# Kernel tuning notes

Measured on AMD Instinct MI355X. Metric: run time of the kernel, lower is better.

Reference implementation:

```python
import jax, jax.numpy as jnp
import numpy as np


def _lin_lrelu(x, W, b):
    # LinearBlock(c_in, c_out): Linear + LeakyReLU(0.01)
    return jax.nn.leaky_relu(x @ W + b)


def _mrconv(x_src, x_dst, edges, index_id, W, b):
    """BipartiteResMRConv: gather-diff-scatter_max + residual MLP.
    x_src: [B, Ns, C], x_dst: [B, Nd, C], edges: [2, E] int."""
    src = index_id[0][edges[0]]                     # [E]
    dst = index_id[0][edges[1]]                     # [E]
    diffs = x_dst[:, dst, :] - x_src[:, src, :]     # [B, E, C]
    d = jnp.swapaxes(diffs, 0, 1)                   # [E, B, C] (segment axis leading)
    m = jax.ops.segment_max(d, dst, num_segments=x_dst.shape[1])  # [Nd, B, C]
    m = jnp.where(jnp.isneginf(m), 0.0, m)          # empty segments -> 0 (maxes init zeros)
    maxes = jnp.swapaxes(m, 0, 1)                   # [B, Nd, C]
    h = jnp.concatenate([x_dst, maxes], axis=2)     # [B, Nd, 2C]
    return x_dst + _lin_lrelu(h, W, b)


def setup_inputs() -> dict:
    key = jax.random.key(0)
    ks = jax.random.split(key, 24)
    B, Nf, Ne, Nv, C = 4, 40000, 80000, 40000, 32
    E_fe, E_ev, E_ff, E_ef, E_ve = 160000, 160000, 240000, 160000, 160000

    def edges(k, E, ns, nd):
        k1, k2 = jax.random.split(k)
        return jnp.stack([jax.random.randint(k1, (E,), 0, ns),
                          jax.random.randint(k2, (E,), 0, nd)]).astype(jnp.int64)

    inp = {
        "x_f": jax.random.normal(ks[0], (B, Nf, 4), jnp.float32),
        "x_e": jax.random.normal(ks[1], (B, Ne, 6), jnp.float32),
        "x_v": jax.random.normal(ks[2], (B, Nv, 3), jnp.float32),
        "index_id": jnp.arange(max(Nf, Ne, Nv), dtype=jnp.int64)[None, :],
        "fe_edges": edges(ks[3], E_fe, Nf, Ne),
        "ev_edges": edges(ks[4], E_ev, Ne, Nv),
        "ff_edges": edges(ks[5], E_ff, Nf, Nf),
        "ef_edges": edges(ks[6], E_ef, Ne, Nf),
        "ve_edges": edges(ks[7], E_ve, Nv, Ne),
        "Wf": jax.random.normal(ks[8], (4, C), jnp.float32) * 0.1,
        "bf": jnp.zeros((C,), jnp.float32),
        "We": jax.random.normal(ks[9], (6, C), jnp.float32) * 0.1,
        "be": jnp.zeros((C,), jnp.float32),
        "Wv": jax.random.normal(ks[10], (3, C), jnp.float32) * 0.1,
        "bv": jnp.zeros((C,), jnp.float32),
    }
    for i, name in enumerate(["f2e", "e2v", "ff", "e2f", "v2e"]):
        inp[f"W_{name}"] = jax.random.normal(ks[11 + i], (2 * C, C), jnp.float32) * 0.1
        inp[f"b_{name}"] = jnp.zeros((C,), jnp.float32)
    return inp


def reference(x_f, x_e, x_v, index_id, fe_edges, ev_edges, ff_edges, ef_edges,
              ve_edges, Wf, bf, We, be, Wv, bv, W_f2e, b_f2e, W_e2v, b_e2v,
              W_ff, b_ff, W_e2f, b_e2f, W_v2e, b_v2e):
    xf0 = _lin_lrelu(x_f, Wf, bf)   # [B, Nf, 32]
    xe0 = _lin_lrelu(x_e, We, be)   # [B, Ne, 32]
    xv0 = _lin_lrelu(x_v, Wv, bv)   # [B, Nv, 32]
    xe = _mrconv(xf0, xe0, fe_edges, index_id, W_f2e, b_f2e)   # F2E
    xv = _mrconv(xe0, xv0, ev_edges, index_id, W_e2v, b_e2v)   # E2V
    xf = _mrconv(xf0, xf0, ff_edges, index_id, W_ff, b_ff)     # F2F (ffLayers)
    xf = _mrconv(xe, xf, ef_edges, index_id, W_e2f, b_e2f)     # E2F
    xe = _mrconv(xv, xe, ve_edges, index_id, W_v2e, b_v2e)     # V2E
    return (xf, xe, xv)
```

## Files before the change

### kernel.cpp

```cpp
#include <hip/hip_runtime.h>
#include <float.h>

#define LRELU(v) ((v) > 0.0f ? (v) : 0.01f * (v))

__device__ __forceinline__ int f2ord(float f) {
    int i = __float_as_int(f);
    return (i >= 0) ? i : (int)(0x80000000u - (unsigned int)i);
}
__device__ __forceinline__ float ord2f(int m) {
    int i = (m >= 0) ? m : (int)(0x80000000u - (unsigned int)m);
    return __int_as_float(i);
}

__global__ void prep(const float* __restrict__ xf, const float* __restrict__ xe,
                     const float* __restrict__ Wf, const float* __restrict__ bf,
                     const float* __restrict__ We, const float* __restrict__ be,
                     float* __restrict__ of, float* __restrict__ oe,
                     const int* __restrict__ e0, const int* __restrict__ e1,
                     const int* __restrict__ e2, const int* __restrict__ e3,
                     const int* __restrict__ e4, int* __restrict__ cur,
                     int* __restrict__ slots) {
    int bid = blockIdx.x;
    int t = threadIdx.x;
    if (bid < 15000) {
        int loc = bid * 256 + t;
        const int QF = 1280000;
        const float* x; const float* W; const float* bb; float* o; int cin;
        if (loc < QF) { x = xf; W = Wf; bb = bf; o = of; cin = 4; }
        else          { x = xe; W = We; bb = be; o = oe; cin = 6; loc -= QF; }
        int c0 = (loc & 7) * 4;
        int r  = loc >> 3;
        float4 acc = *(const float4*)(bb + c0);
        for (int k = 0; k < cin; ++k) {
            float xv_ = x[r * cin + k];
            float4 wv = *(const float4*)(W + k * 32 + c0);
            acc.x = fmaf(xv_, wv.x, acc.x); acc.y = fmaf(xv_, wv.y, acc.y);
            acc.z = fmaf(xv_, wv.z, acc.z); acc.w = fmaf(xv_, wv.w, acc.w);
        }
        float4 ov4;
        ov4.x = LRELU(acc.x); ov4.y = LRELU(acc.y);
        ov4.z = LRELU(acc.z); ov4.w = LRELU(acc.w);
        ((float4*)o)[loc] = ov4;
    } else {
        int idx = (bid - 15000) * 256 + t;
        if (idx >= 880000) return;
        const int cum[6]  = {0, 160000, 320000, 560000, 720000, 880000};
        const int bOff[5] = {0, 2500, 3750, 5000, 6250};
        const int Eg[5]   = {160000, 160000, 240000, 160000, 160000};
        const int* eds[5] = {e0, e1, e2, e3, e4};
        int g = 0;
#pragma unroll
        for (int k = 1; k < 5; ++k) g += (idx >= cum[k]);
        int e = idx - cum[g];
        int s = eds[g][e];
        int d = eds[g][Eg[g] + e];
        int cbase = (bOff[g] + (d >> 5)) * 8 + (idx & 7);
        int c = atomicAdd(&cur[cbase], 1);
        if (c < 64) slots[(size_t)cbase * 64 + c] = (s << 5) | (d & 31);
    }
}

struct ConvJob {
    const float* xsrc; const float* xdst;
    const int* cur; const int* slots;
    const float* W; const float* bias; float* out;
    const float* xraw; const float* Wlin; const float* blin;
    int Ns; int Nd; int blkStart; int cin;
};
struct ConvJobs { ConvJob e[3]; };

__global__ __launch_bounds__(256, 1)
void conv_fused(ConvJobs jobs) {
    __shared__ int smxi[128][33];
    int t = threadIdx.x;
    int bid = blockIdx.x;
    int g = (bid >= jobs.e[2].blkStart) ? 2 : (bid >= jobs.e[1].blkStart) ? 1 : 0;
    const float* xsrc  = jobs.e[g].xsrc;
    const float* xdst  = jobs.e[g].xdst;
    const int*   cur   = jobs.e[g].cur;
    const int*   slots = jobs.e[g].slots;
    const float* W     = jobs.e[g].W;
    const float* bias  = jobs.e[g].bias;
    float*       out   = jobs.e[g].out;
    const float* xraw  = jobs.e[g].xraw;
    const float* Wlin  = jobs.e[g].Wlin;
    const float* blin  = jobs.e[g].blin;
    int Ns = jobs.e[g].Ns, Nd = jobs.e[g].Nd;
    int cin = jobs.e[g].cin;
    int lb = bid - jobs.e[g].blkStart;
    int base = lb * 32;

    for (int i = t; i < 128 * 33; i += 256) ((int*)smxi)[i] = 0x7FFFFFFF;
    __syncthreads();

    int w    = t >> 6;
    int lane = t & 63;
    int r    = (w & 1) * 64 + lane;
    int c0   = __builtin_amdgcn_readfirstlane((w >> 1) * 16);
    int nl = r >> 2, b2 = r & 3;
    int d  = base + nl;
    float xd[32];
    if (cin > 0) {
#pragma unroll
        for (int c = 0; c < 32; ++c) xd[c] = blin[c];
        const float* xrp = xraw + ((size_t)b2 * Nd + d) * cin;
        for (int k = 0; k < cin; ++k) {
            float xrk = xrp[k];
            const float* wk = Wlin + k * 32;
#pragma unroll
            for (int c = 0; c < 32; ++c) xd[c] = fmaf(xrk, wk[c], xd[c]);
        }
#pragma unroll
        for (int c = 0; c < 32; ++c) xd[c] = LRELU(xd[c]);
    } else {
        const float* xdp = xdst + ((size_t)b2 * Nd + d) * 32;
#pragma unroll
        for (int q = 0; q < 8; ++q) {
            float4 v = ((const float4*)xdp)[q];
            xd[4*q] = v.x; xd[4*q+1] = v.y; xd[4*q+2] = v.z; xd[4*q+3] = v.w;
        }
    }

    {
        int c4 = t & 7;
        int b  = (t >> 3) & 3;
        int el = t >> 5;
        int len = cur[lb * 8 + el];
        len = len > 64 ? 64 : len;
        const int* ce = slots + (size_t)(lb * 8 + el) * 64;
        const float* xsb = xsrc + (size_t)b * Ns * 32 + c4 * 4;
        for (int j = 0; j < len; j += 8) {
            int4 sw0 = *(const int4*)(ce + j);
            int4 sw1 = *(const int4*)(ce + j + 4);
            int sea = sw0.x;
            int se1 = (j + 1 < len) ? sw0.y : sea;
            int se2 = (j + 2 < len) ? sw0.z : sea;
            int se3 = (j + 3 < len) ? sw0.w : sea;
            int se4 = (j + 4 < len) ? sw1.x : sea;
            int se5 = (j + 5 < len) ? sw1.y : sea;
            int se6 = (j + 6 < len) ? sw1.z : sea;
            int se7 = (j + 7 < len) ? sw1.w : sea;
            float4 v0 = *(const float4*)(xsb + (size_t)(sea & ~31));
            float4 v1 = *(const float4*)(xsb + (size_t)(se1 & ~31));
            float4 v2 = *(const float4*)(xsb + (size_t)(se2 & ~31));
            float4 v3 = *(const float4*)(xsb + (size_t)(se3 & ~31));
            float4 v4 = *(const float4*)(xsb + (size_t)(se4 & ~31));
            float4 v5 = *(const float4*)(xsb + (size_t)(se5 & ~31));
            float4 v6 = *(const float4*)(xsb + (size_t)(se6 & ~31));
            float4 v7 = *(const float4*)(xsb + (size_t)(se7 & ~31));
#define MINGRP(se, v)  { int* mr = &smxi[((se) & 31) * 4 + b][c4 * 4]; \
            atomicMin(&mr[0], f2ord((v).x)); atomicMin(&mr[1], f2ord((v).y)); \
            atomicMin(&mr[2], f2ord((v).z)); atomicMin(&mr[3], f2ord((v).w)); }
            MINGRP(sea, v0) MINGRP(se1, v1) MINGRP(se2, v2) MINGRP(se3, v3)
            MINGRP(se4, v4) MINGRP(se5, v5) MINGRP(se6, v6) MINGRP(se7, v7)
#undef MINGRP
        }
    }
    __syncthreads();

    bool has = (smxi[r][0] != 0x7FFFFFFF);
    float mx[32];
#pragma unroll
    for (int q = 0; q < 32; ++q) {
        int iv = smxi[r][q];
        mx[q] = has ? (xd[q] - ord2f(iv)) : 0.0f;
    }
    const float* Wc = W + c0;
    float acc[16];
#pragma unroll
    for (int jj = 0; jj < 16; ++jj) acc[jj] = bias[c0 + jj];
#pragma unroll
    for (int k = 0; k < 64; ++k) {
        float hk = (k < 32) ? xd[k] : mx[k - 32];
        const float4* wr = (const float4*)(Wc + k * 32);
        float4 w0 = wr[0], w1 = wr[1], w2 = wr[2], w3 = wr[3];
        acc[0]  = fmaf(hk, w0.x, acc[0]);  acc[1]  = fmaf(hk, w0.y, acc[1]);
        acc[2]  = fmaf(hk, w0.z, acc[2]);  acc[3]  = fmaf(hk, w0.w, acc[3]);
        acc[4]  = fmaf(hk, w1.x, acc[4]);  acc[5]  = fmaf(hk, w1.y, acc[5]);
        acc[6]  = fmaf(hk, w1.z, acc[6]);  acc[7]  = fmaf(hk, w1.w, acc[7]);
        acc[8]  = fmaf(hk, w2.x, acc[8]);  acc[9]  = fmaf(hk, w2.y, acc[9]);
        acc[10] = fmaf(hk, w2.z, acc[10]); acc[11] = fmaf(hk, w2.w, acc[11]);
        acc[12] = fmaf(hk, w3.x, acc[12]); acc[13] = fmaf(hk, w3.y, acc[13]);
        acc[14] = fmaf(hk, w3.z, acc[14]); acc[15] = fmaf(hk, w3.w, acc[15]);
    }
    float xr[16];
#pragma unroll
    for (int i = 0; i < 16; ++i) xr[i] = (c0 == 0) ? xd[i] : xd[16 + i];
    float* op = out + ((size_t)b2 * Nd + d) * 32 + c0;
#pragma unroll
    for (int q = 0; q < 4; ++q) {
        float4 o;
        float a0 = acc[4*q], a1 = acc[4*q+1], a2 = acc[4*q+2], a3 = acc[4*q+3];
        o.x = xr[4*q]   + LRELU(a0); o.y = xr[4*q+1] + LRELU(a1);
        o.z = xr[4*q+2] + LRELU(a2); o.w = xr[4*q+3] + LRELU(a3);
        ((float4*)op)[q] = o;
    }
}

extern "C" void kernel_launch(void* const* d_in, const int* in_sizes, int n_in,
                              void* d_out, int out_size, void* d_ws, size_t ws_size,
                              hipStream_t stream) {
    const float* x_f = (const float*)d_in[0];
    const float* x_e = (const float*)d_in[1];
    const float* x_v = (const float*)d_in[2];
    const int* fe = (const int*)d_in[4];
    const int* ev = (const int*)d_in[5];
    const int* ff = (const int*)d_in[6];
    const int* ef = (const int*)d_in[7];
    const int* ve = (const int*)d_in[8];
    const float* Wf = (const float*)d_in[9];
    const float* bf = (const float*)d_in[10];
    const float* We = (const float*)d_in[11];
    const float* be = (const float*)d_in[12];
    const float* Wv = (const float*)d_in[13];
    const float* bv = (const float*)d_in[14];
    const float* W_f2e = (const float*)d_in[15];
    const float* b_f2e = (const float*)d_in[16];
    const float* W_e2v = (const float*)d_in[17];
    const float* b_e2v = (const float*)d_in[18];
    const float* W_ff  = (const float*)d_in[19];
    const float* b_ff  = (const float*)d_in[20];
    const float* W_e2f = (const float*)d_in[21];
    const float* b_e2f = (const float*)d_in[22];
    const float* W_v2e = (const float*)d_in[23];
    const float* b_v2e = (const float*)d_in[24];

    const int B = 4, Nf = 40000, Ne = 80000, Nv = 40000;
    const int NFC = B * Nf * 32;
    const int NEC = B * Ne * 32;
    const int CUR_TOTAL = 70016;
    const int SLOT_TOTAL = 8750 * 512;
    const int INT_WORDS = CUR_TOTAL + SLOT_TOTAL;

    float* oxf = (float*)d_out;
    float* oxe = oxf + NFC;
    float* oxv = oxe + NEC;

    size_t needA = (size_t)(NFC + 2 * NEC) * 4 + (size_t)INT_WORDS * 4;
    bool merged = ws_size >= needA;

    float* ws  = (float*)d_ws;
    float* xf0 = ws;
    float* xe0 = ws + NFC;
    float* xe1 = merged ? (ws + NFC + NEC) : oxe;
    int* cur   = (int*)(merged ? (ws + NFC + 2 * NEC) : (ws + NFC + NEC));
    int* slots = cur + CUR_TOTAL;

    hipMemsetAsync(cur, 0, (size_t)CUR_TOTAL * 4, stream);

    prep<<<15000 + 3438, 256, 0, stream>>>(
        x_f, x_e, Wf, bf, We, be, xf0, xe0,
        fe, ev, ff, ef, ve, cur, slots);

    const int* cu_f2e = cur;            const int* sl_f2e = slots;
    const int* cu_e2v = cur + 2500*8;   const int* sl_e2v = slots + (size_t)2500*512;
    const int* cu_ff  = cur + 3750*8;   const int* sl_ff  = slots + (size_t)3750*512;
    const int* cu_e2f = cur + 5000*8;   const int* sl_e2f = slots + (size_t)5000*512;
    const int* cu_v2e = cur + 6250*8;   const int* sl_v2e = slots + (size_t)6250*512;

    {
        ConvJobs j;
        j.e[0] = {xf0, xe0, cu_f2e, sl_f2e, W_f2e, b_f2e, xe1,
                  nullptr, nullptr, nullptr, Nf, Ne, 0, 0};
        j.e[1] = {xe0, oxv, cu_e2v, sl_e2v, W_e2v, b_e2v, oxv,
                  x_v, Wv, bv, Ne, Nv, 2500, 3};
        j.e[2] = {xf0, xf0, cu_ff,  sl_ff,  W_ff,  b_ff,  oxf,
                  nullptr, nullptr, nullptr, Nf, Nf, 3750, 0};
        conv_fused<<<5000, 256, 0, stream>>>(j);
    }
    if (merged) {
        ConvJobs j;
        j.e[0] = {xe1, oxf, cu_e2f, sl_e2f, W_e2f, b_e2f, oxf,
                  nullptr, nullptr, nullptr, Ne, Nf, 0, 0};
        j.e[1] = {oxv, xe1, cu_v2e, sl_v2e, W_v2e, b_v2e, oxe,
                  nullptr, nullptr, nullptr, Nv, Ne, 1250, 0};
        j.e[2] = j.e[0]; j.e[2].blkStart = 0x7FFFFFFF;
        conv_fused<<<3750, 256, 0, stream>>>(j);
    } else {
        {
            ConvJobs j;
            j.e[0] = {oxe, oxf, cu_e2f, sl_e2f, W_e2f, b_e2f, oxf,
                      nullptr, nullptr, nullptr, Ne, Nf, 0, 0};
            j.e[1] = j.e[0]; j.e[1].blkStart = 0x7FFFFFFF;
            j.e[2] = j.e[0]; j.e[2].blkStart = 0x7FFFFFFF;
            conv_fused<<<1250, 256, 0, stream>>>(j);
        }
        {
            ConvJobs j;
            j.e[0] = {oxv, oxe, cu_v2e, sl_v2e, W_v2e, b_v2e, oxe,
                      nullptr, nullptr, nullptr, Nv, Ne, 0, 0};
            j.e[1] = j.e[0]; j.e[1].blkStart = 0x7FFFFFFF;
            j.e[2] = j.e[0]; j.e[2].blkStart = 0x7FFFFFFF;
            conv_fused<<<2500, 256, 0, stream>>>(j);
        }
    }
}
```

Baseline: 379.5 us.

## Fuse input linear layers into conv gather, recompute source features on the fly

Removes the separate precompute of xf0/xe0 in the prep kernel. The first conv launch now recomputes the small input Linear+LeakyReLU (cin 4 or 6) per gathered edge from the raw inputs, and per destination node for xdst. Gathering 16–24 raw bytes per edge replaces 128-byte feature rows and avoids writing and re-reading the intermediate tensors, at the cost of redundant FMAs per edge. Workspace needs shrink as a side effect.

```diff
diff --git a/kernel.cpp b/kernel.cpp
--- a/kernel.cpp
+++ b/kernel.cpp
@@ -12,60 +12,34 @@
     return __int_as_float(i);
 }
 
-__global__ void prep(const float* __restrict__ xf, const float* __restrict__ xe,
-                     const float* __restrict__ Wf, const float* __restrict__ bf,
-                     const float* __restrict__ We, const float* __restrict__ be,
-                     float* __restrict__ of, float* __restrict__ oe,
-                     const int* __restrict__ e0, const int* __restrict__ e1,
+__global__ void prep(const int* __restrict__ e0, const int* __restrict__ e1,
                      const int* __restrict__ e2, const int* __restrict__ e3,
                      const int* __restrict__ e4, int* __restrict__ cur,
                      int* __restrict__ slots) {
-    int bid = blockIdx.x;
-    int t = threadIdx.x;
-    if (bid < 15000) {
-        int loc = bid * 256 + t;
-        const int QF = 1280000;
-        const float* x; const float* W; const float* bb; float* o; int cin;
-        if (loc < QF) { x = xf; W = Wf; bb = bf; o = of; cin = 4; }
-        else          { x = xe; W = We; bb = be; o = oe; cin = 6; loc -= QF; }
-        int c0 = (loc & 7) * 4;
-        int r  = loc >> 3;
-        float4 acc = *(const float4*)(bb + c0);
-        for (int k = 0; k < cin; ++k) {
-            float xv_ = x[r * cin + k];
-            float4 wv = *(const float4*)(W + k * 32 + c0);
-            acc.x = fmaf(xv_, wv.x, acc.x); acc.y = fmaf(xv_, wv.y, acc.y);
-            acc.z = fmaf(xv_, wv.z, acc.z); acc.w = fmaf(xv_, wv.w, acc.w);
-        }
-        float4 ov4;
-        ov4.x = LRELU(acc.x); ov4.y = LRELU(acc.y);
-        ov4.z = LRELU(acc.z); ov4.w = LRELU(acc.w);
-        ((float4*)o)[loc] = ov4;
-    } else {
-        int idx = (bid - 15000) * 256 + t;
-        if (idx >= 880000) return;
-        const int cum[6]  = {0, 160000, 320000, 560000, 720000, 880000};
-        const int bOff[5] = {0, 2500, 3750, 5000, 6250};
-        const int Eg[5]   = {160000, 160000, 240000, 160000, 160000};
-        const int* eds[5] = {e0, e1, e2, e3, e4};
-        int g = 0;
-#pragma unroll
-        for (int k = 1; k < 5; ++k) g += (idx >= cum[k]);
-        int e = idx - cum[g];
-        int s = eds[g][e];
-        int d = eds[g][Eg[g] + e];
-        int cbase = (bOff[g] + (d >> 5)) * 8 + (idx & 7);
-        int c = atomicAdd(&cur[cbase], 1);
-        if (c < 64) slots[(size_t)cbase * 64 + c] = (s << 5) | (d & 31);
-    }
+    int idx = blockIdx.x * 256 + threadIdx.x;
+    if (idx >= 880000) return;
+    const int cum[6]  = {0, 160000, 320000, 560000, 720000, 880000};
+    const int bOff[5] = {0, 2500, 3750, 5000, 6250};
+    const int Eg[5]   = {160000, 160000, 240000, 160000, 160000};
+    const int* eds[5] = {e0, e1, e2, e3, e4};
+    int g = 0;
+#pragma unroll
+    for (int k = 1; k < 5; ++k) g += (idx >= cum[k]);
+    int e = idx - cum[g];
+    int s = eds[g][e];
+    int d = eds[g][Eg[g] + e];
+    int cbase = (bOff[g] + (d >> 5)) * 8 + (idx & 7);
+    int c = atomicAdd(&cur[cbase], 1);
+    if (c < 64) slots[(size_t)cbase * 64 + c] = (s << 5) | (d & 31);
 }
 
 struct ConvJob {
     const float* xsrc; const float* xdst;
     const int* cur; const int* slots;
     const float* W; const float* bias; float* out;
-    const float* xraw; const float* Wlin; const float* blin;
-    int Ns; int Nd; int blkStart; int cin;
+    const float* sraw; const float* sW; const float* sb; int scin;
+    const float* draw; const float* dW; const float* db; int dcin;
+    int Ns; int Nd; int blkStart;
 };
 struct ConvJobs { ConvJob e[3]; };
 
@@ -82,11 +56,15 @@
     const float* W     = jobs.e[g].W;
     const float* bias  = jobs.e[g].bias;
     float*       out   = jobs.e[g].out;
-    const float* xraw  = jobs.e[g].xraw;
-    const float* Wlin  = jobs.e[g].Wlin;
-    const float* blin  = jobs.e[g].blin;
+    const float* sraw  = jobs.e[g].sraw;
+    const float* sW    = jobs.e[g].sW;
+    const float* sb    = jobs.e[g].sb;
+    int scin           = jobs.e[g].scin;
+    const float* draw  = jobs.e[g].draw;
+    const float* dW    = jobs.e[g].dW;
+    const float* db    = jobs.e[g].db;
+    int dcin           = jobs.e[g].dcin;
     int Ns = jobs.e[g].Ns, Nd = jobs.e[g].Nd;
-    int cin = jobs.e[g].cin;
     int lb = bid - jobs.e[g].blkStart;
     int base = lb * 32;
 
@@ -100,13 +78,13 @@
     int nl = r >> 2, b2 = r & 3;
     int d  = base + nl;
     float xd[32];
-    if (cin > 0) {
-#pragma unroll
-        for (int c = 0; c < 32; ++c) xd[c] = blin[c];
-        const float* xrp = xraw + ((size_t)b2 * Nd + d) * cin;
-        for (int k = 0; k < cin; ++k) {
+    if (dcin > 0) {
+#pragma unroll
+        for (int c = 0; c < 32; ++c) xd[c] = db[c];
+        const float* xrp = draw + ((size_t)b2 * Nd + d) * dcin;
+        for (int k = 0; k < dcin; ++k) {
             float xrk = xrp[k];
-            const float* wk = Wlin + k * 32;
+            const float* wk = dW + k * 32;
 #pragma unroll
             for (int c = 0; c < 32; ++c) xd[c] = fmaf(xrk, wk[c], xd[c]);
         }
@@ -128,32 +106,106 @@
         int len = cur[lb * 8 + el];
         len = len > 64 ? 64 : len;
         const int* ce = slots + (size_t)(lb * 8 + el) * 64;
-        const float* xsb = xsrc + (size_t)b * Ns * 32 + c4 * 4;
-        for (int j = 0; j < len; j += 8) {
-            int4 sw0 = *(const int4*)(ce + j);
-            int4 sw1 = *(const int4*)(ce + j + 4);
-            int sea = sw0.x;
-            int se1 = (j + 1 < len) ? sw0.y : sea;
-            int se2 = (j + 2 < len) ? sw0.z : sea;
-            int se3 = (j + 3 < len) ? sw0.w : sea;
-            int se4 = (j + 4 < len) ? sw1.x : sea;
-            int se5 = (j + 5 < len) ? sw1.y : sea;
-            int se6 = (j + 6 < len) ? sw1.z : sea;
-            int se7 = (j + 7 < len) ? sw1.w : sea;
-            float4 v0 = *(const float4*)(xsb + (size_t)(sea & ~31));
-            float4 v1 = *(const float4*)(xsb + (size_t)(se1 & ~31));
-            float4 v2 = *(const float4*)(xsb + (size_t)(se2 & ~31));
-            float4 v3 = *(const float4*)(xsb + (size_t)(se3 & ~31));
-            float4 v4 = *(const float4*)(xsb + (size_t)(se4 & ~31));
-            float4 v5 = *(const float4*)(xsb + (size_t)(se5 & ~31));
-            float4 v6 = *(const float4*)(xsb + (size_t)(se6 & ~31));
-            float4 v7 = *(const float4*)(xsb + (size_t)(se7 & ~31));
+        if (scin == 0) {
+            const float* xsb = xsrc + (size_t)b * Ns * 32 + c4 * 4;
+            for (int j = 0; j < len; j += 8) {
+                int4 sw0 = *(const int4*)(ce + j);
+                int4 sw1 = *(const int4*)(ce + j + 4);
+                int sea = sw0.x;
+                int se1 = (j + 1 < len) ? sw0.y : sea;
+                int se2 = (j + 2 < len) ? sw0.z : sea;
+                int se3 = (j + 3 < len) ? sw0.w : sea;
+                int se4 = (j + 4 < len) ? sw1.x : sea;
+                int se5 = (j + 5 < len) ? sw1.y : sea;
+                int se6 = (j + 6 < len) ? sw1.z : sea;
+                int se7 = (j + 7 < len) ? sw1.w : sea;
+                float4 v0 = *(const float4*)(xsb + (size_t)(sea & ~31));
+                float4 v1 = *(const float4*)(xsb + (size_t)(se1 & ~31));
+                float4 v2 = *(const float4*)(xsb + (size_t)(se2 & ~31));
+                float4 v3 = *(const float4*)(xsb + (size_t)(se3 & ~31));
+                float4 v4 = *(const float4*)(xsb + (size_t)(se4 & ~31));
+                float4 v5 = *(const float4*)(xsb + (size_t)(se5 & ~31));
+                float4 v6 = *(const float4*)(xsb + (size_t)(se6 & ~31));
+                float4 v7 = *(const float4*)(xsb + (size_t)(se7 & ~31));
 #define MINGRP(se, v)  { int* mr = &smxi[((se) & 31) * 4 + b][c4 * 4]; \
-            atomicMin(&mr[0], f2ord((v).x)); atomicMin(&mr[1], f2ord((v).y)); \
-            atomicMin(&mr[2], f2ord((v).z)); atomicMin(&mr[3], f2ord((v).w)); }
-            MINGRP(sea, v0) MINGRP(se1, v1) MINGRP(se2, v2) MINGRP(se3, v3)
-            MINGRP(se4, v4) MINGRP(se5, v5) MINGRP(se6, v6) MINGRP(se7, v7)
-#undef MINGRP
+                atomicMin(&mr[0], f2ord((v).x)); atomicMin(&mr[1], f2ord((v).y)); \
+                atomicMin(&mr[2], f2ord((v).z)); atomicMin(&mr[3], f2ord((v).w)); }
+                MINGRP(sea, v0) MINGRP(se1, v1) MINGRP(se2, v2) MINGRP(se3, v3)
+                MINGRP(se4, v4) MINGRP(se5, v5) MINGRP(se6, v6) MINGRP(se7, v7)
+            }
+        } else if (scin == 4) {
+            const float* xr = sraw + (size_t)b * Ns * 4;
+            float4 w0 = *(const float4*)(sW +  0 + c4 * 4);
+            float4 w1 = *(const float4*)(sW + 32 + c4 * 4);
+            float4 w2 = *(const float4*)(sW + 64 + c4 * 4);
+            float4 w3 = *(const float4*)(sW + 96 + c4 * 4);
+            float4 bq = *(const float4*)(sb + c4 * 4);
+            for (int j = 0; j < len; j += 8) {
+                int4 sw0 = *(const int4*)(ce + j);
+                int4 sw1 = *(const int4*)(ce + j + 4);
+                int sea = sw0.x;
+                int se1 = (j + 1 < len) ? sw0.y : sea;
+                int se2 = (j + 2 < len) ? sw0.z : sea;
+                int se3 = (j + 3 < len) ? sw0.w : sea;
+                int se4 = (j + 4 < len) ? sw1.x : sea;
+                int se5 = (j + 5 < len) ? sw1.y : sea;
+                int se6 = (j + 6 < len) ? sw1.z : sea;
+                int se7 = (j + 7 < len) ? sw1.w : sea;
+                float4 r0 = *(const float4*)(xr + (size_t)(sea >> 5) * 4);
+                float4 r1 = *(const float4*)(xr + (size_t)(se1 >> 5) * 4);
+                float4 r2 = *(const float4*)(xr + (size_t)(se2 >> 5) * 4);
+                float4 r3 = *(const float4*)(xr + (size_t)(se3 >> 5) * 4);
+                float4 r4 = *(const float4*)(xr + (size_t)(se4 >> 5) * 4);
+                float4 r5 = *(const float4*)(xr + (size_t)(se5 >> 5) * 4);
+                float4 r6 = *(const float4*)(xr + (size_t)(se6 >> 5) * 4);
+                float4 r7 = *(const float4*)(xr + (size_t)(se7 >> 5) * 4);
+#define CMIN4(se, rr) { \
+    float vx = fmaf((rr).w, w3.x, fmaf((rr).z, w2.x, fmaf((rr).y, w1.x, fmaf((rr).x, w0.x, bq.x)))); \
+    float vy = fmaf((rr).w, w3.y, fmaf((rr).z, w2.y, fmaf((rr).y, w1.y, fmaf((rr).x, w0.y, bq.y)))); \
+    float vz = fmaf((rr).w, w3.z, fmaf((rr).z, w2.z, fmaf((rr).y, w1.z, fmaf((rr).x, w0.z, bq.z)))); \
+    float vw = fmaf((rr).w, w3.w, fmaf((rr).z, w2.w, fmaf((rr).y, w1.w, fmaf((rr).x, w0.w, bq.w)))); \
+    vx = LRELU(vx); vy = LRELU(vy); vz = LRELU(vz); vw = LRELU(vw); \
+    int* mr = &smxi[((se) & 31) * 4 + b][c4 * 4]; \
+    atomicMin(&mr[0], f2ord(vx)); atomicMin(&mr[1], f2ord(vy)); \
+    atomicMin(&mr[2], f2ord(vz)); atomicMin(&mr[3], f2ord(vw)); }
+                CMIN4(sea, r0) CMIN4(se1, r1) CMIN4(se2, r2) CMIN4(se3, r3)
+                CMIN4(se4, r4) CMIN4(se5, r5) CMIN4(se6, r6) CMIN4(se7, r7)
+            }
+        } else {
+            const float* xr = sraw + (size_t)b * Ns * 6;
+            float4 w0 = *(const float4*)(sW +   0 + c4 * 4);
+            float4 w1 = *(const float4*)(sW +  32 + c4 * 4);
+            float4 w2 = *(const float4*)(sW +  64 + c4 * 4);
+            float4 w3 = *(const float4*)(sW +  96 + c4 * 4);
+            float4 w4 = *(const float4*)(sW + 128 + c4 * 4);
+            float4 w5 = *(const float4*)(sW + 160 + c4 * 4);
+            float4 bq = *(const float4*)(sb + c4 * 4);
+            for (int j = 0; j < len; j += 4) {
+                int4 sw0 = *(const int4*)(ce + j);
+                int sea = sw0.x;
+                int se1 = (j + 1 < len) ? sw0.y : sea;
+                int se2 = (j + 2 < len) ? sw0.z : sea;
+                int se3 = (j + 3 < len) ? sw0.w : sea;
+                const float* p0 = xr + (size_t)(sea >> 5) * 6;
+                const float* p1 = xr + (size_t)(se1 >> 5) * 6;
+                const float* p2 = xr + (size_t)(se2 >> 5) * 6;
+                const float* p3 = xr + (size_t)(se3 >> 5) * 6;
+                float2 a0 = *(const float2*)p0, b0 = *(const float2*)(p0 + 2), c0_ = *(const float2*)(p0 + 4);
+                float2 a1 = *(const float2*)p1, b1 = *(const float2*)(p1 + 2), c1_ = *(const float2*)(p1 + 4);
+                float2 a2 = *(const float2*)p2, b2_ = *(const float2*)(p2 + 2), c2_ = *(const float2*)(p2 + 4);
+                float2 a3 = *(const float2*)p3, b3 = *(const float2*)(p3 + 2), c3_ = *(const float2*)(p3 + 4);
+#define CMIN6(se, A, Bv, Cv) { \
+    float vx = fmaf((Cv).y, w5.x, fmaf((Cv).x, w4.x, fmaf((Bv).y, w3.x, fmaf((Bv).x, w2.x, fmaf((A).y, w1.x, fmaf((A).x, w0.x, bq.x)))))); \
+    float vy = fmaf((Cv).y, w5.y, fmaf((Cv).x, w4.y, fmaf((Bv).y, w3.y, fmaf((Bv).x, w2.y, fmaf((A).y, w1.y, fmaf((A).x, w0.y, bq.y)))))); \
+    float vz = fmaf((Cv).y, w5.z, fmaf((Cv).x, w4.z, fmaf((Bv).y, w3.z, fmaf((Bv).x, w2.z, fmaf((A).y, w1.z, fmaf((A).x, w0.z, bq.z)))))); \
+    float vw = fmaf((Cv).y, w5.w, fmaf((Cv).x, w4.w, fmaf((Bv).y, w3.w, fmaf((Bv).x, w2.w, fmaf((A).y, w1.w, fmaf((A).x, w0.w, bq.w)))))); \
+    vx = LRELU(vx); vy = LRELU(vy); vz = LRELU(vz); vw = LRELU(vw); \
+    int* mr = &smxi[((se) & 31) * 4 + b][c4 * 4]; \
+    atomicMin(&mr[0], f2ord(vx)); atomicMin(&mr[1], f2ord(vy)); \
+    atomicMin(&mr[2], f2ord(vz)); atomicMin(&mr[3], f2ord(vw)); }
+                CMIN6(sea, a0, b0, c0_) CMIN6(se1, a1, b1, c1_)
+                CMIN6(se2, a2, b2_, c2_) CMIN6(se3, a3, b3, c3_)
+            }
         }
     }
     __syncthreads();
@@ -173,26 +225,26 @@
     for (int k = 0; k < 64; ++k) {
         float hk = (k < 32) ? xd[k] : mx[k - 32];
         const float4* wr = (const float4*)(Wc + k * 32);
-        float4 w0 = wr[0], w1 = wr[1], w2 = wr[2], w3 = wr[3];
-        acc[0]  = fmaf(hk, w0.x, acc[0]);  acc[1]  = fmaf(hk, w0.y, acc[1]);
-        acc[2]  = fmaf(hk, w0.z, acc[2]);  acc[3]  = fmaf(hk, w0.w, acc[3]);
-        acc[4]  = fmaf(hk, w1.x, acc[4]);  acc[5]  = fmaf(hk, w1.y, acc[5]);
-        acc[6]  = fmaf(hk, w1.z, acc[6]);  acc[7]  = fmaf(hk, w1.w, acc[7]);
-        acc[8]  = fmaf(hk, w2.x, acc[8]);  acc[9]  = fmaf(hk, w2.y, acc[9]);
-        acc[10] = fmaf(hk, w2.z, acc[10]); acc[11] = fmaf(hk, w2.w, acc[11]);
-        acc[12] = fmaf(hk, w3.x, acc[12]); acc[13] = fmaf(hk, w3.y, acc[13]);
-        acc[14] = fmaf(hk, w3.z, acc[14]); acc[15] = fmaf(hk, w3.w, acc[15]);
-    }
-    float xr[16];
-#pragma unroll
-    for (int i = 0; i < 16; ++i) xr[i] = (c0 == 0) ? xd[i] : xd[16 + i];
+        float4 q0 = wr[0], q1 = wr[1], q2 = wr[2], q3 = wr[3];
+        acc[0]  = fmaf(hk, q0.x, acc[0]);  acc[1]  = fmaf(hk, q0.y, acc[1]);
+        acc[2]  = fmaf(hk, q0.z, acc[2]);  acc[3]  = fmaf(hk, q0.w, acc[3]);
+        acc[4]  = fmaf(hk, q1.x, acc[4]);  acc[5]  = fmaf(hk, q1.y, acc[5]);
+        acc[6]  = fmaf(hk, q1.z, acc[6]);  acc[7]  = fmaf(hk, q1.w, acc[7]);
+        acc[8]  = fmaf(hk, q2.x, acc[8]);  acc[9]  = fmaf(hk, q2.y, acc[9]);
+        acc[10] = fmaf(hk, q2.z, acc[10]); acc[11] = fmaf(hk, q2.w, acc[11]);
+        acc[12] = fmaf(hk, q3.x, acc[12]); acc[13] = fmaf(hk, q3.y, acc[13]);
+        acc[14] = fmaf(hk, q3.z, acc[14]); acc[15] = fmaf(hk, q3.w, acc[15]);
+    }
+    float xr2[16];
+#pragma unroll
+    for (int i = 0; i < 16; ++i) xr2[i] = (c0 == 0) ? xd[i] : xd[16 + i];
     float* op = out + ((size_t)b2 * Nd + d) * 32 + c0;
 #pragma unroll
     for (int q = 0; q < 4; ++q) {
         float4 o;
         float a0 = acc[4*q], a1 = acc[4*q+1], a2 = acc[4*q+2], a3 = acc[4*q+3];
-        o.x = xr[4*q]   + LRELU(a0); o.y = xr[4*q+1] + LRELU(a1);
-        o.z = xr[4*q+2] + LRELU(a2); o.w = xr[4*q+3] + LRELU(a3);
+        o.x = xr2[4*q]   + LRELU(a0); o.y = xr2[4*q+1] + LRELU(a1);
+        o.z = xr2[4*q+2] + LRELU(a2); o.w = xr2[4*q+3] + LRELU(a3);
         ((float4*)op)[q] = o;
     }
 }
@@ -236,21 +288,17 @@
     float* oxe = oxf + NFC;
     float* oxv = oxe + NEC;
 
-    size_t needA = (size_t)(NFC + 2 * NEC) * 4 + (size_t)INT_WORDS * 4;
+    size_t needA = (size_t)NEC * 4 + (size_t)INT_WORDS * 4;
     bool merged = ws_size >= needA;
 
     float* ws  = (float*)d_ws;
-    float* xf0 = ws;
-    float* xe0 = ws + NFC;
-    float* xe1 = merged ? (ws + NFC + NEC) : oxe;
-    int* cur   = (int*)(merged ? (ws + NFC + 2 * NEC) : (ws + NFC + NEC));
+    float* xe1 = merged ? ws : oxe;
+    int* cur   = (int*)(merged ? (ws + NEC) : ws);
     int* slots = cur + CUR_TOTAL;
 
     hipMemsetAsync(cur, 0, (size_t)CUR_TOTAL * 4, stream);
 
-    prep<<<15000 + 3438, 256, 0, stream>>>(
-        x_f, x_e, Wf, bf, We, be, xf0, xe0,
-        fe, ev, ff, ef, ve, cur, slots);
+    prep<<<3438, 256, 0, stream>>>(fe, ev, ff, ef, ve, cur, slots);
 
     const int* cu_f2e = cur;            const int* sl_f2e = slots;
     const int* cu_e2v = cur + 2500*8;   const int* sl_e2v = slots + (size_t)2500*512;
@@ -260,27 +308,30 @@
 
     {
         ConvJobs j;
-        j.e[0] = {xf0, xe0, cu_f2e, sl_f2e, W_f2e, b_f2e, xe1,
-                  nullptr, nullptr, nullptr, Nf, Ne, 0, 0};
-        j.e[1] = {xe0, oxv, cu_e2v, sl_e2v, W_e2v, b_e2v, oxv,
-                  x_v, Wv, bv, Ne, Nv, 2500, 3};
-        j.e[2] = {xf0, xf0, cu_ff,  sl_ff,  W_ff,  b_ff,  oxf,
-                  nullptr, nullptr, nullptr, Nf, Nf, 3750, 0};
+        j.e[0] = {nullptr, nullptr, cu_f2e, sl_f2e, W_f2e, b_f2e, xe1,
+                  x_f, Wf, bf, 4,  x_e, We, be, 6,  Nf, Ne, 0};
+        j.e[1] = {nullptr, nullptr, cu_e2v, sl_e2v, W_e2v, b_e2v, oxv,
+                  x_e, We, be, 6,  x_v, Wv, bv, 3,  Ne, Nv, 2500};
+        j.e[2] = {nullptr, nullptr, cu_ff,  sl_ff,  W_ff,  b_ff,  oxf,
+                  x_f, Wf, bf, 4,  x_f, Wf, bf, 4,  Nf, Nf, 3750};
         conv_fused<<<5000, 256, 0, stream>>>(j);
     }
     if (merged) {
         ConvJobs j;
         j.e[0] = {xe1, oxf, cu_e2f, sl_e2f, W_e2f, b_e2f, oxf,
-                  nullptr, nullptr, nullptr, Ne, Nf, 0, 0};
+                  nullptr, nullptr, nullptr, 0, nullptr, nullptr, nullptr, 0,
+                  Ne, Nf, 0};
         j.e[1] = {oxv, xe1, cu_v2e, sl_v2e, W_v2e, b_v2e, oxe,
-                  nullptr, nullptr, nullptr, Nv, Ne, 1250, 0};
+                  nullptr, nullptr, nullptr, 0, nullptr, nullptr, nullptr, 0,
+                  Nv, Ne, 1250};
         j.e[2] = j.e[0]; j.e[2].blkStart = 0x7FFFFFFF;
         conv_fused<<<3750, 256, 0, stream>>>(j);
     } else {
         {
             ConvJobs j;
             j.e[0] = {oxe, oxf, cu_e2f, sl_e2f, W_e2f, b_e2f, oxf,
-                      nullptr, nullptr, nullptr, Ne, Nf, 0, 0};
+                      nullptr, nullptr, nullptr, 0, nullptr, nullptr, nullptr, 0,
+                      Ne, Nf, 0};
             j.e[1] = j.e[0]; j.e[1].blkStart = 0x7FFFFFFF;
             j.e[2] = j.e[0]; j.e[2].blkStart = 0x7FFFFFFF;
             conv_fused<<<1250, 256, 0, stream>>>(j);
@@ -288,7 +339,8 @@
         {
             ConvJobs j;
             j.e[0] = {oxv, oxe, cu_v2e, sl_v2e, W_v2e, b_v2e, oxe,
-                      nullptr, nullptr, nullptr, Nv, Ne, 0, 0};
+                      nullptr, nullptr, nullptr, 0, nullptr, nullptr, nullptr, 0,
+                      Nv, Ne, 0};
             j.e[1] = j.e[0]; j.e[1].blkStart = 0x7FFFFFFF;
             j.e[2] = j.e[0]; j.e[2].blkStart = 0x7FFFFFFF;
             conv_fused<<<2500, 256, 0, stream>>>(j);
```

After: 351.5 us. 7.4% less time.
